# Optimization experiments

Measured on AMD Instinct MI355X. Metric: run time of the kernel, lower is better.

Reference implementation:

```python
import jax, jax.numpy as jnp
import numpy as np

N, DEG, C, D = 4096, 12, 4, 2
E = N * DEG
P = 2 * (D + 1) ** 2          # 18 radial MLPs: value set (s=0) + attention-key set (s=1)
R_MAX = (2 * D + 1) * C * C   # largest radial output size = 80


def _ln(x, g, b, eps=1e-5):
    mu = jnp.mean(x, axis=-1, keepdims=True)
    var = jnp.mean((x - mu) ** 2, axis=-1, keepdims=True)
    return (x - mu) / jnp.sqrt(var + eps) * g + b


def setup_inputs() -> dict:
    key = jax.random.key(0)
    ks = jax.random.split(key, 40)
    inp = {}
    inp["u"] = jax.random.randint(ks[0], (E,), 0, N)   # src nodes
    inp["v"] = jnp.repeat(jnp.arange(N), DEG)           # dst nodes: every node has DEG in-edges
    inp["dist"] = jax.random.uniform(ks[1], (E,))
    for k in range(D + 1):
        inp[f"f{k}"] = jax.random.normal(ks[2 + k], (N, C, 2 * k + 1))
    i = 5
    for k in range(D + 1):
        for l in range(D + 1):
            J = 2 * min(k, l) + 1
            inp[f"wj_{k}{l}"] = jax.random.normal(ks[i], (E, J, 2 * l + 1, 2 * k + 1)) * 0.2
            i += 1
    inp["wq"] = jax.random.normal(ks[i], (D + 1, C, C)) * 0.4; i += 1
    inp["rad_W1"] = jax.random.normal(ks[i], (P, 16, C + 1)) * 0.3; i += 1
    inp["rad_b1"] = jnp.zeros((P, 16)); inp["rad_g1"] = jnp.ones((P, 16)); inp["rad_be1"] = jnp.zeros((P, 16))
    inp["rad_W2"] = jax.random.normal(ks[i], (P, 16, 16)) * 0.25; i += 1
    inp["rad_b2"] = jnp.zeros((P, 16)); inp["rad_g2"] = jnp.ones((P, 16)); inp["rad_be2"] = jnp.zeros((P, 16))
    inp["rad_W3"] = jax.random.normal(ks[i], (P, R_MAX, 16)) * 0.2; i += 1
    inp["rad_b3"] = jnp.zeros((P, R_MAX))
    inp["si_W1"] = jax.random.normal(ks[i], (D + 1, C * C, C * C)) * 0.25; i += 1
    inp["si_b1"] = jnp.zeros((D + 1, C * C)); inp["si_g1"] = jnp.ones((D + 1, C * C)); inp["si_be1"] = jnp.zeros((D + 1, C * C))
    inp["si_W2"] = jax.random.normal(ks[i], (D + 1, C * C, C * C)) * 0.25; i += 1
    inp["si_b2"] = jnp.zeros((D + 1, C * C)); inp["si_g2"] = jnp.ones((D + 1, C * C)); inp["si_be2"] = jnp.zeros((D + 1, C * C))
    inp["si_W3"] = jax.random.normal(ks[i], (D + 1, C * C, C * C)) * 0.25; i += 1
    inp["si_b3"] = jnp.zeros((D + 1, C * C))
    return inp


def _forward(u, v, dist, f0, f1, f2,
             wj_00, wj_01, wj_02, wj_10, wj_11, wj_12, wj_20, wj_21, wj_22,
             wq, rad_W1, rad_b1, rad_g1, rad_be1, rad_W2, rad_b2, rad_g2, rad_be2, rad_W3, rad_b3,
             si_W1, si_b1, si_g1, si_be1, si_W2, si_b2, si_g2, si_be2, si_W3, si_b3):
    f = [f0, f1, f2]
    wj = {(0, 0): wj_00, (0, 1): wj_01, (0, 2): wj_02,
          (1, 0): wj_10, (1, 1): wj_11, (1, 2): wj_12,
          (2, 0): wj_20, (2, 1): wj_21, (2, 2): wj_22}
    n = f0.shape[0]
    # shared radial input: per-channel <f0_u, f0_v> plus edge distance -> [E, C+1]
    iv = jnp.concatenate([jnp.sum(f0[u] * f0[v], axis=2), dist[:, None]], axis=1)

    def radial(p, J):
        r_size = J * C * C
        h = jax.nn.relu(_ln(iv @ rad_W1[p].T + rad_b1[p], rad_g1[p], rad_be1[p]))
        h = jax.nn.relu(_ln(h @ rad_W2[p].T + rad_b2[p], rad_g2[p], rad_be2[p]))
        return h @ rad_W3[p, :r_size].T + rad_b3[p, :r_size]

    def make_w(k, l, s):
        # WLayer: radial MLP -> [E, J, c_out, c_in], contracted with CG basis w_j
        J = 2 * min(k, l) + 1
        p = s * (D + 1) ** 2 + k * (D + 1) + l
        Rm = radial(p, J).reshape(-1, J, C, C)
        return jnp.einsum('ejoi,ejlk->eoilk', Rm, wj[(k, l)])  # [E,o,i,2l+1,2k+1]

    # --- attention (AttnBlock) ---
    q = jnp.concatenate([jnp.einsum('oi,nik->nok', wq[k], f[k]) for k in range(D + 1)], axis=2)  # [N,C,9]
    k_edge = jnp.concatenate([
        sum(jnp.einsum('eoilk,eik->eol', make_w(k, l, 1), f[k][v]) for k in range(D + 1))
        for l in range(D + 1)], axis=2)  # [E,C,9] (keys use dst features, as in calc_k)
    dot = jnp.einsum('eol,eol->e', q[v], k_edge)
    m = jax.ops.segment_max(dot, v, num_segments=n)
    lse = m + jnp.log(jax.ops.segment_sum(jnp.exp(dot - m[v]), v, num_segments=n))
    a = jnp.exp(dot - lse[v])  # edge softmax over incoming edges of each dst node

    # --- attention-weighted tensor-product messages + scatter-sum (update_all) ---
    outs = []
    for l in range(D + 1):
        vl = sum(jnp.einsum('e,eoilk,eik->eol', a, make_w(k, l, 0), f[k][u]) for k in range(D + 1))
        outs.append(jax.ops.segment_sum(vl, v, num_segments=n))  # [N,C,2l+1]

    # --- self-interaction ---
    for l in range(D + 1):
        inner = jnp.einsum('ncl,ndl->ncd', f[l], f[l]).reshape(n, C * C)
        h = jax.nn.relu(_ln(inner @ si_W1[l].T + si_b1[l], si_g1[l], si_be1[l]))
        h = jax.nn.relu(_ln(h @ si_W2[l].T + si_b2[l], si_g2[l], si_be2[l]))
        siw = (h @ si_W3[l].T + si_b3[l]).reshape(n, C, C)
        outs[l] = outs[l] + jnp.einsum('noi,nil->nol', siw, f[l])

    # concat degree outputs f_out[0..2] along the m-axis -> [N, C, 1+3+5]
    return jnp.concatenate(outs, axis=2)


def reference(u, v, dist, f0, f1, f2,
              wj_00, wj_01, wj_02, wj_10, wj_11, wj_12, wj_20, wj_21, wj_22,
              wq, rad_W1, rad_b1, rad_g1, rad_be1, rad_W2, rad_b2, rad_g2, rad_be2, rad_W3, rad_b3,
              si_W1, si_b1, si_g1, si_be1, si_W2, si_b2, si_g2, si_be2, si_W3, si_b3):
    return _forward(u, v, dist, f0, f1, f2,
                    wj_00, wj_01, wj_02, wj_10, wj_11, wj_12, wj_20, wj_21, wj_22,
                    wq, rad_W1, rad_b1, rad_g1, rad_be1, rad_W2, rad_b2, rad_g2, rad_be2, rad_W3, rad_b3,
                    si_W1, si_b1, si_g1, si_be1, si_W2, si_b2, si_g2, si_be2, si_W3, si_b3)
```

## Files before the change

### kernel.cpp

```cpp
#include <hip/hip_runtime.h>
#include <hip/hip_bf16.h>

#define DEG 12

typedef short short8v __attribute__((ext_vector_type(8)));
typedef float float4v __attribute__((ext_vector_type(4)));

struct GP {
  const int* u;
  const void* dist;
  const void* f0; const void* f1; const void* f2;
  const void* wj[9];
  const void* wq;
  const void *rW1,*rb1,*rg1,*rbe1,*rW2,*rb2,*rg2,*rbe2,*rW3,*rb3;
  const void *sW1,*sb1,*sg1,*sbe1,*sW2,*sb2,*sg2,*sbe2,*sW3,*sb3;
  void* out;
  const float* wsf;
  const unsigned short* wA;
};

#define WS_W1   0
#define WS_W2   1440
#define WS_W3   6048
#define WS_SI1  29088
#define WS_SI2  29856
#define WS_SI3  30624
#define WS_G1   31392
#define WS_BE1  31680
#define WS_G2   31968
#define WS_BE2  32256
#define WS_B1   32544
#define WS_B2   32832
#define WS_B3   33120
#define WS_TOTAL 34560
#define WS_A_HALF 19456

struct alignas(16) Smem {
  float sRm[DEG][308];
  float sG[DEG][276];
  union {
    float sH2[DEG][148];
    unsigned short sB[9][4][16][4];
  };
  float sF[13][36];
  float sIv[DEG][5];
  float sQ[36];
  float sDot[DEG];
  float sA[DEG];
  float sVl[DEG][36];
  float sSIin[48], sSIh[48], sSIh2[48], sSiw[48];
};

__device__ __forceinline__ float ldv(const __hip_bfloat16* p, int i){ return __bfloat162float(p[i]); }
__device__ __forceinline__ float ldv(const float* p, int i){ return p[i]; }

__device__ __forceinline__ void load16(const __hip_bfloat16* ptr, float* out){
  const uint4* q = reinterpret_cast<const uint4*>(ptr);
  uint4 a = q[0]; uint4 b = q[1];
  unsigned w[8] = {a.x,a.y,a.z,a.w,b.x,b.y,b.z,b.w};
  #pragma unroll
  for (int i=0;i<8;i++){
    out[2*i]   = __uint_as_float(w[i] << 16);
    out[2*i+1] = __uint_as_float(w[i] & 0xffff0000u);
  }
}
__device__ __forceinline__ void load16(const float* ptr, float* out){
  const float4* q = reinterpret_cast<const float4*>(ptr);
  #pragma unroll
  for (int i=0;i<4;i++){
    float4 a = q[i];
    out[4*i]=a.x; out[4*i+1]=a.y; out[4*i+2]=a.z; out[4*i+3]=a.w;
  }
}

__device__ __forceinline__ void st(__hip_bfloat16* p, int i, float v){ p[i] = __float2bfloat16(v); }
__device__ __forceinline__ void st(float* p, int i, float v){ p[i] = v; }

__device__ __forceinline__ unsigned short f2bf(float v){
  __hip_bfloat16 b = __float2bfloat16(v);
  return *reinterpret_cast<unsigned short*>(&b);
}

template<typename WT>
__device__ __forceinline__ void ln_relu16(float* h, const WT* g, const WT* be){
  float mu = 0.f;
  #pragma unroll
  for (int c=0;c<16;c++) mu += h[c];
  mu *= 0.0625f;
  float var = 0.f;
  #pragma unroll
  for (int c=0;c<16;c++){ float d=h[c]-mu; var += d*d; }
  var *= 0.0625f;
  float inv = rsqrtf(var + 1e-5f);
  #pragma unroll
  for (int c=0;c<16;c++){
    float y = (h[c]-mu)*inv*ldv(g,c) + ldv(be,c);
    h[c] = fmaxf(y, 0.f);
  }
}

template<typename WT>
struct WPtr {
  const WT *w1,*w2,*w3,*si1,*si2,*si3,*g1,*be1,*g2,*be2,*b1,*b2,*b3;
};

template<typename WT>
__device__ __forceinline__ void radial12(int S, const WPtr<WT>& W, int t, Smem& s, bool mf){
  const int pk = t/12, e = t%12;
  const int pp = S*9 + pk;
  const float x0=s.sIv[e][0],x1=s.sIv[e][1],x2=s.sIv[e][2],x3=s.sIv[e][3],x4=s.sIv[e][4];
  float h[16];
  #pragma unroll
  for (int r=0;r<16;r++){
    const WT* row = W.w1 + (pp*16+r)*5;
    h[r] = ldv(W.b1,pp*16+r) + ldv(row,0)*x0 + ldv(row,1)*x1
         + ldv(row,2)*x2 + ldv(row,3)*x3 + ldv(row,4)*x4;
  }
  ln_relu16(h, W.g1+pp*16, W.be1+pp*16);
  float h2[16];
  #pragma unroll
  for (int r=0;r<16;r++){
    float wf[16]; load16(W.w2 + (pp*16+r)*16, wf);
    float acc = ldv(W.b2,pp*16+r);
    #pragma unroll
    for (int c=0;c<16;c++) acc += wf[c]*h[c];
    h2[r]=acc;
  }
  ln_relu16(h2, W.g2+pp*16, W.be2+pp*16);
  if (mf){
    #pragma unroll
    for (int c=0;c<16;c++) s.sB[pk][c>>2][e][c&3] = f2bf(h2[c]);
  } else {
    float4* dst = (float4*)&s.sH2[e][pk*16];
    #pragma unroll
    for (int i=0;i<4;i++) dst[i] = make_float4(h2[4*i],h2[4*i+1],h2[4*i+2],h2[4*i+3]);
  }
}

template<typename WT>
__device__ __forceinline__ void radial3(int S, const WPtr<WT>& W, int t, Smem& s){
  const int rq = t/3, eq = t%3;
  const int rflat = rq*4;
  constexpr int RS[10]={0,16,32,48,64,112,160,176,224,304};
  int kp=0;
  #pragma unroll
  for (int k=1;k<9;k++) if (rflat >= RS[k]) kp = k;
  const int rl = rflat - RS[kp];
  const int pp = S*9 + kp;
  const int wbase = (pp*80 + rl)*16;
  float b[4];
  #pragma unroll
  for (int r=0;r<4;r++) b[r] = ldv(W.b3, pp*80+rl+r);
  #pragma unroll
  for (int half=0; half<2; ++half){
    const int e0 = eq*4 + half*2, e1 = e0+1;
    const float4* hp0 = (const float4*)&s.sH2[e0][kp*16];
    const float4* hp1 = (const float4*)&s.sH2[e1][kp*16];
    float4 ha[4], hb[4];
    #pragma unroll
    for (int i=0;i<4;i++){ ha[i]=hp0[i]; hb[i]=hp1[i]; }
    float a0[4], a1[4];
    #pragma unroll
    for (int r=0;r<4;r++){
      float wf[16]; load16(W.w3 + wbase + r*16, wf);
      float s0=0.f, s1=0.f;
      const float* h0 = (const float*)&ha[0];
      const float* h1 = (const float*)&hb[0];
      #pragma unroll
      for (int c=0;c<16;c++){ s0 += wf[c]*h0[c]; s1 += wf[c]*h1[c]; }
      a0[r]=b[r]+s0; a1[r]=b[r]+s1;
    }
    *(float4*)&s.sRm[e0][rflat] = make_float4(a0[0],a0[1],a0[2],a0[3]);
    *(float4*)&s.sRm[e1][rflat] = make_float4(a1[0],a1[1],a1[2],a1[3]);
  }
}

__device__ __forceinline__ void radial3_mfma(int S, const float* wsf,
                                             const unsigned short* wA, int t, Smem& s){
  const int wave = t>>6, lane = t&63;
  const int col = lane&15, kq = lane>>4;
  #pragma unroll
  for (int t5=0; t5<5; ++t5){
    const int tile = wave + t5*4;
    if (tile < 19){
      const int rflat = tile*16;
      int kp=0;
      if (rflat>=16)  kp=1;
      if (rflat>=32)  kp=2;
      if (rflat>=48)  kp=3;
      if (rflat>=64)  kp=4;
      if (rflat>=112) kp=5;
      if (rflat>=160) kp=6;
      if (rflat>=176) kp=7;
      if (rflat>=224) kp=8;
      const int rs = (kp==0)?0:(kp==1)?16:(kp==2)?32:(kp==3)?48:(kp==4)?64:(kp==5)?112:(kp==6)?160:(kp==7)?176:224;
      const int rl = rflat - rs;
      const int pp = S*9 + kp;
      short8v a = *reinterpret_cast<const short8v*>(wA + (size_t)(S*19+tile)*512 + (size_t)lane*8);
      const unsigned short* bp = &s.sB[kp][kq][col][0];
      short4 blo = *reinterpret_cast<const short4*>(bp);
      short8v b;
      b[0]=blo.x; b[1]=blo.y; b[2]=blo.z; b[3]=blo.w;
      b[4]=blo.x; b[5]=blo.y; b[6]=blo.z; b[7]=blo.w;
      float4v c; c[0]=0.f; c[1]=0.f; c[2]=0.f; c[3]=0.f;
      float4v d = __builtin_amdgcn_mfma_f32_16x16x32_bf16(a, b, c, 0, 0, 0);
      if (col < 12){
        const float4 bb = *reinterpret_cast<const float4*>(wsf + WS_B3 + pp*80 + rl + kq*4);
        *(float4*)&s.sRm[col][rflat + kq*4] =
          make_float4(d[0]+bb.x, d[1]+bb.y, d[2]+bb.z, d[3]+bb.w);
      }
    }
  }
}

template<typename T>
__device__ __forceinline__ void stage_g(int S, const GP& p, int tt, int n12, Smem& s){
  constexpr int GOFF[9]={0,4,16,36,40,76,136,140,176};
  #pragma unroll
  for (int kp=0;kp<9;kp++){
    const int kk=kp/3, ll=kp%3;
    const int mn = kk<ll?kk:ll;
    const int J=2*mn+1, Lm=2*ll+1, Km=2*kk+1;
    const int koff = (kk==0)?0:((kk==1)?4:16);
    const int goff = GOFF[kp];
    const T* wjp = (const T*)p.wj[kp];
    const int nt = 12*J*Lm;
    for (int q=tt; q<nt; q+=128){
      int e = q/(J*Lm), jl = q%(J*Lm);
      int j = jl/Lm, lm = jl%Lm;
      const T* w = wjp + ((size_t)((n12+e)*J + j)*Lm + lm)*Km;
      const float* fv = S ? &s.sF[12][koff] : &s.sF[e][koff];
      float a0=0.f,a1=0.f,a2=0.f,a3=0.f;
      #pragma unroll
      for (int km=0;km<Km;km++){
        float wv = ldv(w,km);
        a0 += wv*fv[0*Km+km];
        a1 += wv*fv[1*Km+km];
        a2 += wv*fv[2*Km+km];
        a3 += wv*fv[3*Km+km];
      }
      float* gd = &s.sG[e][goff];
      gd[(j*4+0)*Lm+lm]=a0;
      gd[(j*4+1)*Lm+lm]=a1;
      gd[(j*4+2)*Lm+lm]=a2;
      gd[(j*4+3)*Lm+lm]=a3;
    }
  }
}

template<typename T, typename WT>
__device__ void gconv_run(const GP& p, Smem& s, const WPtr<WT>& W, bool mf){
  const int n = blockIdx.x;
  const int t = threadIdx.x;
  const int n12 = n*DEG;
  const T* f0=(const T*)p.f0; const T* f1=(const T*)p.f1; const T* f2=(const T*)p.f2;
  constexpr int ROFF[9]={0,16,32,48,64,112,160,176,224};
  constexpr int GOFF[9]={0,4,16,36,40,76,136,140,176};

  for (int q0=t; q0<13*36; q0+=256){
    int node=q0/36, j=q0%36;
    int idn = (node<DEG)? p.u[n12+node] : n;
    float v;
    if (j<4)       v = ldv(f0, idn*4  + j);
    else if (j<16) v = ldv(f1, idn*12 + (j-4));
    else           v = ldv(f2, idn*20 + (j-16));
    s.sF[node][j] = v;
  }
  __syncthreads();

  if (t<48){ int e=t>>2, c=t&3; s.sIv[e][c] = s.sF[e][c]*s.sF[12][c]; }
  else if (t<60){ int e=t-48; s.sIv[e][4] = ldv((const T*)p.dist, n12+e); }
  else if (t>=64 && t<100){
    int t2=t-64, o=t2/9, mc=t2%9;
    int k = (mc<1)?0:((mc<4)?1:2);
    int m = mc - ((k==0)?0:((k==1)?1:4));
    int koff=(k==0)?0:((k==1)?4:16), Km=2*k+1;
    float acc=0.f;
    #pragma unroll
    for (int i=0;i<4;i++) acc += ldv((const T*)p.wq,(k*4+o)*4+i) * s.sF[12][koff+i*Km+m];
    s.sQ[t2]=acc;
  } else if (t>=128 && t<176){
    int t3=t-128, l=t3/16, rr=t3%16, o=rr>>2, i=rr&3;
    int koff=(l==0)?0:((l==1)?4:16), Lm=2*l+1;
    float acc=0.f;
    for (int m=0;m<Lm;m++) acc += s.sF[12][koff+o*Lm+m]*s.sF[12][koff+i*Lm+m];
    s.sSIin[t3]=acc;
  }
  __syncthreads();

  if (t<108)       radial12(1, W, t, s, mf);
  else if (t>=128) stage_g<T>(1, p, t-128, n12, s);
  __syncthreads();

  if (mf)          radial3_mfma(1, p.wsf, p.wA, t, s);
  else if (t<228)  radial3(1, W, t, s);
  __syncthreads();

  if (t<192){
    const int e=t>>4, o=(t>>2)&3, i=t&3;
    float d=0.f;
    #pragma unroll
    for (int kp=0;kp<9;kp++){
      const int kk=kp/3, ll=kp%3;
      const int mn=kk<ll?kk:ll;
      const int J=2*mn+1, Lm=2*ll+1;
      const int loff=(ll==0)?0:((ll==1)?1:4);
      #pragma unroll
      for (int j=0;j<J;j++){
        float rm = s.sRm[e][ROFF[kp]+j*16+o*4+i];
        #pragma unroll
        for (int lm=0;lm<Lm;lm++)
          d += rm * s.sG[e][GOFF[kp]+(j*4+i)*Lm+lm] * s.sQ[o*9+loff+lm];
      }
    }
    d += __shfl_xor(d,1);
    d += __shfl_xor(d,2);
    d += __shfl_xor(d,4);
    d += __shfl_xor(d,8);
    if ((t&15)==0) s.sDot[e]=d;
  } else if (t<240){
    int idx=t-192, l=idx/16, r=idx%16;
    float wf[16]; load16(W.si1 + (l*16+r)*16, wf);
    float acc = ldv((const T*)p.sb1,l*16+r);
    #pragma unroll
    for (int c=0;c<16;c++) acc += wf[c]*s.sSIin[l*16+c];
    s.sSIh[idx]=acc;
  }
  __syncthreads();

  if (t<108)       radial12(0, W, t, s, mf);
  else if (t==127){
    float mx=-1e30f;
    #pragma unroll
    for (int e=0;e<12;e++) mx = fmaxf(mx, s.sDot[e]);
    float ex[12]; float se=0.f;
    #pragma unroll
    for (int e=0;e<12;e++){ ex[e]=__expf(s.sDot[e]-mx); se += ex[e]; }
    #pragma unroll
    for (int e=0;e<12;e++) s.sA[e] = ex[e]/se;
  }
  else if (t>=128) stage_g<T>(0, p, t-128, n12, s);
  __syncthreads();

  if (mf)          radial3_mfma(0, p.wsf, p.wA, t, s);
  else if (t<228)  radial3(0, W, t, s);
  __syncthreads();

  if (t>=64){
    for (int q=t-64; q<432; q+=192){
      int l,e,o,lm;
      if (q<48){ l=0; e=q>>2; o=q&3; lm=0; }
      else if (q<192){ int r=q-48; l=1; e=r/12; int r2=r%12; o=r2/3; lm=r2%3; }
      else { int r=q-192; l=2; e=r/20; int r2=r%20; o=r2/5; lm=r2%5; }
      const int Lm=2*l+1, loff=(l==0)?0:((l==1)?1:4);
      float acc=0.f;
      for (int kk=0;kk<3;kk++){
        const int kp=kk*3+l;
        const int mn=kk<l?kk:l;
        const int J=2*mn+1;
        for (int j=0;j<J;j++)
          #pragma unroll
          for (int i=0;i<4;i++)
            acc += s.sRm[e][ROFF[kp]+j*16+o*4+i] * s.sG[e][GOFF[kp]+(j*4+i)*Lm+lm];
      }
      s.sVl[e][o*9+loff+lm]=acc;
    }
  } else if (t<48){
    int l=t/16, r=t%16;
    float mu=0.f;
    #pragma unroll
    for (int c=0;c<16;c++) mu += s.sSIh[l*16+c];
    mu *= 0.0625f;
    float var=0.f;
    #pragma unroll
    for (int c=0;c<16;c++){ float d=s.sSIh[l*16+c]-mu; var+=d*d; }
    var *= 0.0625f;
    float inv = rsqrtf(var+1e-5f);
    float wf[16]; load16(W.si2 + (l*16+r)*16, wf);
    float acc = ldv((const T*)p.sb2,l*16+r);
    #pragma unroll
    for (int c=0;c<16;c++){
      float y = (s.sSIh[l*16+c]-mu)*inv*ldv((const T*)p.sg1,l*16+c) + ldv((const T*)p.sbe1,l*16+c);
      acc += wf[c]*fmaxf(y,0.f);
    }
    s.sSIh2[t]=acc;
  }
  __syncthreads();

  if (t<48){
    int l=t/16, r=t%16;
    float mu=0.f;
    #pragma unroll
    for (int c=0;c<16;c++) mu += s.sSIh2[l*16+c];
    mu *= 0.0625f;
    float var=0.f;
    #pragma unroll
    for (int c=0;c<16;c++){ float d=s.sSIh2[l*16+c]-mu; var+=d*d; }
    var *= 0.0625f;
    float inv = rsqrtf(var+1e-5f);
    float wf[16]; load16(W.si3 + (l*16+r)*16, wf);
    float acc = ldv((const T*)p.sb3,l*16+r);
    #pragma unroll
    for (int c=0;c<16;c++){
      float y = (s.sSIh2[l*16+c]-mu)*inv*ldv((const T*)p.sg2,l*16+c) + ldv((const T*)p.sbe2,l*16+c);
      acc += wf[c]*fmaxf(y,0.f);
    }
    s.sSiw[t]=acc;
  }
  __syncthreads();

  if (t<36){
    int o=t/9, mc=t%9;
    int l = (mc<1)?0:((mc<4)?1:2);
    int m = mc - ((l==0)?0:((l==1)?1:4));
    int koff=(l==0)?0:((l==1)?4:16), Lm=2*l+1;
    float acc=0.f;
    #pragma unroll
    for (int e=0;e<12;e++) acc += s.sA[e]*s.sVl[e][t];
    #pragma unroll
    for (int i=0;i<4;i++) acc += s.sSiw[l*16+o*4+i]*s.sF[12][koff+i*Lm+m];
    st((T*)p.out, n*36+t, acc);
  }
}

template<typename T>
__device__ __forceinline__ void gconv_dispatch(const GP& p, Smem& s){
  if (p.wsf){
    const float* w = p.wsf;
    WPtr<float> W{w+WS_W1, w+WS_W2, w+WS_W3, w+WS_SI1, w+WS_SI2, w+WS_SI3,
                  w+WS_G1, w+WS_BE1, w+WS_G2, w+WS_BE2, w+WS_B1, w+WS_B2, w+WS_B3};
    gconv_run<T,float>(p, s, W, p.wA != nullptr);
  } else {
    WPtr<T> W{(const T*)p.rW1,(const T*)p.rW2,(const T*)p.rW3,
              (const T*)p.sW1,(const T*)p.sW2,(const T*)p.sW3,
              (const T*)p.rg1,(const T*)p.rbe1,(const T*)p.rg2,(const T*)p.rbe2,
              (const T*)p.rb1,(const T*)p.rb2,(const T*)p.rb3};
    gconv_run<T,T>(p, s, W, false);
  }
}

__global__ __launch_bounds__(256,4) void gconv_kernel(GP p){
  __shared__ Smem s;
  const unsigned magic = *(const unsigned*)p.rg1;
  if (magic == 0x3F803F80u) gconv_dispatch<__hip_bfloat16>(p, s);
  else                      gconv_dispatch<float>(p, s);
}

template<typename T>
__device__ __forceinline__ void prep_body(const GP& p, float* ws, int i){
  float v;
  if      (i<WS_W2)  v = ldv((const T*)p.rW1,  i-WS_W1);
  else if (i<WS_W3)  v = ldv((const T*)p.rW2,  i-WS_W2);
  else if (i<WS_SI1) v = ldv((const T*)p.rW3,  i-WS_W3);
  else if (i<WS_SI2) v = ldv((const T*)p.sW1,  i-WS_SI1);
  else if (i<WS_SI3) v = ldv((const T*)p.sW2,  i-WS_SI2);
  else if (i<WS_G1)  v = ldv((const T*)p.sW3,  i-WS_SI3);
  else if (i<WS_BE1) v = ldv((const T*)p.rg1,  i-WS_G1);
  else if (i<WS_G2)  v = ldv((const T*)p.rbe1, i-WS_BE1);
  else if (i<WS_BE2) v = ldv((const T*)p.rg2,  i-WS_G2);
  else if (i<WS_B1)  v = ldv((const T*)p.rbe2, i-WS_BE2);
  else if (i<WS_B2)  v = ldv((const T*)p.rb1,  i-WS_B1);
  else if (i<WS_B3)  v = ldv((const T*)p.rb2,  i-WS_B2);
  else               v = ldv((const T*)p.rb3,  i-WS_B3);
  ws[i] = v;
}

__global__ void prep_kernel(GP p, float* ws){
  int i = blockIdx.x*256 + threadIdx.x;
  if (i >= WS_TOTAL) return;
  const unsigned magic = *(const unsigned*)p.rg1;
  if (magic == 0x3F803F80u) prep_body<__hip_bfloat16>(p, ws, i);
  else                      prep_body<float>(p, ws, i);
}

__global__ void prep2_kernel(GP p, unsigned short* wsA){
  int i = blockIdx.x*256 + threadIdx.x;
  if (i >= 2*19*512) return;
  const unsigned magic = *(const unsigned*)p.rg1;
  int st   = i>>9;
  int lane = (i>>3)&63;
  int j    = i&7;
  int S = st/19, tile = st%19;
  int rflat = tile*16;
  int kp=0;
  if (rflat>=16)  kp=1;
  if (rflat>=32)  kp=2;
  if (rflat>=48)  kp=3;
  if (rflat>=64)  kp=4;
  if (rflat>=112) kp=5;
  if (rflat>=160) kp=6;
  if (rflat>=176) kp=7;
  if (rflat>=224) kp=8;
  const int rs = (kp==0)?0:(kp==1)?16:(kp==2)?32:(kp==3)?48:(kp==4)?64:(kp==5)?112:(kp==6)?160:(kp==7)?176:224;
  const int rl = rflat - rs;
  const int pp = S*9 + kp;
  const int row = lane&15;
  const int k = 4*(lane>>4) + (j&3);
  float v = 0.f;
  if (j < 4){
    int idx = (pp*80 + rl + row)*16 + k;
    v = (magic==0x3F803F80u) ? ldv((const __hip_bfloat16*)p.rW3, idx)
                             : ldv((const float*)p.rW3, idx);
  }
  wsA[i] = f2bf(v);
}

extern "C" void kernel_launch(void* const* d_in, const int* in_sizes, int n_in,
                              void* d_out, int out_size, void* d_ws, size_t ws_size,
                              hipStream_t stream) {
  GP p;
  p.u    = (const int*)d_in[0];
  p.dist = d_in[2];
  p.f0   = d_in[3];
  p.f1   = d_in[4];
  p.f2   = d_in[5];
  for (int kp=0;kp<9;kp++) p.wj[kp] = d_in[6+kp];
  p.wq   = d_in[15];
  p.rW1  = d_in[16]; p.rb1  = d_in[17]; p.rg1  = d_in[18]; p.rbe1 = d_in[19];
  p.rW2  = d_in[20]; p.rb2  = d_in[21]; p.rg2  = d_in[22]; p.rbe2 = d_in[23];
  p.rW3  = d_in[24]; p.rb3  = d_in[25];
  p.sW1  = d_in[26]; p.sb1  = d_in[27]; p.sg1  = d_in[28]; p.sbe1 = d_in[29];
  p.sW2  = d_in[30]; p.sb2  = d_in[31]; p.sg2  = d_in[32]; p.sbe2 = d_in[33];
  p.sW3  = d_in[34]; p.sb3  = d_in[35];
  p.out  = d_out;

  const bool use_ws = (ws_size >= (size_t)WS_TOTAL*sizeof(float));
  const bool use_mf = (ws_size >= (size_t)WS_TOTAL*sizeof(float) + (size_t)WS_A_HALF*sizeof(unsigned short));
  p.wsf = use_ws ? (const float*)d_ws : nullptr;
  unsigned short* wsA = use_mf ? (unsigned short*)((float*)d_ws + WS_TOTAL) : nullptr;
  p.wA = wsA;

  if (use_ws)
    prep_kernel<<<dim3((WS_TOTAL+255)/256), dim3(256), 0, stream>>>(p, (float*)d_ws);
  if (use_mf)
    prep2_kernel<<<dim3((2*19*512+255)/256), dim3(256), 0, stream>>>(p, wsA);
  gconv_kernel<<<dim3(4096), dim3(256), 0, stream>>>(p);
}
```

Before: 258.5 us.

## Fuse radial MFMA output with attention-dot and value contraction, split MFMA kernel

Adds a separate MFMA-path kernel that no longer writes the radial weights to shared memory. It contracts the MFMA results directly with the basis products in registers, accumulating the attention logits (key set) and the per-edge values (value set) with LDS atomics. The self-interaction MLP steps are spread across otherwise idle threads of the existing stages, which removes separate passes and barriers. Dropping the large sRm and sH2 buffers shrinks the shared-memory footprint, which may allow more resident blocks, at the cost of LDS atomic contention and a duplicated fallback kernel.

```diff
diff --git a/kernel.cpp b/kernel.cpp
--- a/kernel.cpp
+++ b/kernel.cpp
@@ -35,20 +35,16 @@
 #define WS_TOTAL 34560
 #define WS_A_HALF 19456
 
-struct alignas(16) Smem {
-  float sRm[DEG][308];
+struct alignas(16) SmemM {
   float sG[DEG][276];
-  union {
-    float sH2[DEG][148];
-    unsigned short sB[9][4][16][4];
-  };
   float sF[13][36];
+  float sVl[DEG][36];
   float sIv[DEG][5];
   float sQ[36];
   float sDot[DEG];
   float sA[DEG];
-  float sVl[DEG][36];
-  float sSIin[48], sSIh[48], sSIh2[48], sSiw[48];
+  float sSIa[48], sSIb[48];
+  unsigned short sB[2][9][4][16][4];
 };
 
 __device__ __forceinline__ float ldv(const __hip_bfloat16* p, int i){ return __bfloat162float(p[i]); }
@@ -104,81 +100,38 @@
   const WT *w1,*w2,*w3,*si1,*si2,*si3,*g1,*be1,*g2,*be2,*b1,*b2,*b3;
 };
 
-template<typename WT>
-__device__ __forceinline__ void radial12(int S, const WPtr<WT>& W, int t, Smem& s, bool mf){
+
+__device__ __forceinline__ void radial12m(int S, const WPtr<float>& W, int t, SmemM& s){
   const int pk = t/12, e = t%12;
   const int pp = S*9 + pk;
   const float x0=s.sIv[e][0],x1=s.sIv[e][1],x2=s.sIv[e][2],x3=s.sIv[e][3],x4=s.sIv[e][4];
   float h[16];
   #pragma unroll
   for (int r=0;r<16;r++){
-    const WT* row = W.w1 + (pp*16+r)*5;
-    h[r] = ldv(W.b1,pp*16+r) + ldv(row,0)*x0 + ldv(row,1)*x1
-         + ldv(row,2)*x2 + ldv(row,3)*x3 + ldv(row,4)*x4;
+    const float* row = W.w1 + (pp*16+r)*5;
+    h[r] = W.b1[pp*16+r] + row[0]*x0 + row[1]*x1 + row[2]*x2 + row[3]*x3 + row[4]*x4;
   }
   ln_relu16(h, W.g1+pp*16, W.be1+pp*16);
   float h2[16];
   #pragma unroll
   for (int r=0;r<16;r++){
     float wf[16]; load16(W.w2 + (pp*16+r)*16, wf);
-    float acc = ldv(W.b2,pp*16+r);
+    float acc = W.b2[pp*16+r];
     #pragma unroll
     for (int c=0;c<16;c++) acc += wf[c]*h[c];
     h2[r]=acc;
   }
   ln_relu16(h2, W.g2+pp*16, W.be2+pp*16);
-  if (mf){
-    #pragma unroll
-    for (int c=0;c<16;c++) s.sB[pk][c>>2][e][c&3] = f2bf(h2[c]);
-  } else {
-    float4* dst = (float4*)&s.sH2[e][pk*16];
-    #pragma unroll
-    for (int i=0;i<4;i++) dst[i] = make_float4(h2[4*i],h2[4*i+1],h2[4*i+2],h2[4*i+3]);
-  }
-}
-
-template<typename WT>
-__device__ __forceinline__ void radial3(int S, const WPtr<WT>& W, int t, Smem& s){
-  const int rq = t/3, eq = t%3;
-  const int rflat = rq*4;
-  constexpr int RS[10]={0,16,32,48,64,112,160,176,224,304};
-  int kp=0;
-  #pragma unroll
-  for (int k=1;k<9;k++) if (rflat >= RS[k]) kp = k;
-  const int rl = rflat - RS[kp];
-  const int pp = S*9 + kp;
-  const int wbase = (pp*80 + rl)*16;
-  float b[4];
-  #pragma unroll
-  for (int r=0;r<4;r++) b[r] = ldv(W.b3, pp*80+rl+r);
-  #pragma unroll
-  for (int half=0; half<2; ++half){
-    const int e0 = eq*4 + half*2, e1 = e0+1;
-    const float4* hp0 = (const float4*)&s.sH2[e0][kp*16];
-    const float4* hp1 = (const float4*)&s.sH2[e1][kp*16];
-    float4 ha[4], hb[4];
-    #pragma unroll
-    for (int i=0;i<4;i++){ ha[i]=hp0[i]; hb[i]=hp1[i]; }
-    float a0[4], a1[4];
-    #pragma unroll
-    for (int r=0;r<4;r++){
-      float wf[16]; load16(W.w3 + wbase + r*16, wf);
-      float s0=0.f, s1=0.f;
-      const float* h0 = (const float*)&ha[0];
-      const float* h1 = (const float*)&hb[0];
-      #pragma unroll
-      for (int c=0;c<16;c++){ s0 += wf[c]*h0[c]; s1 += wf[c]*h1[c]; }
-      a0[r]=b[r]+s0; a1[r]=b[r]+s1;
-    }
-    *(float4*)&s.sRm[e0][rflat] = make_float4(a0[0],a0[1],a0[2],a0[3]);
-    *(float4*)&s.sRm[e1][rflat] = make_float4(a1[0],a1[1],a1[2],a1[3]);
-  }
-}
-
-__device__ __forceinline__ void radial3_mfma(int S, const float* wsf,
-                                             const unsigned short* wA, int t, Smem& s){
+  #pragma unroll
+  for (int c=0;c<16;c++) s.sB[S][pk][c>>2][e][c&3] = f2bf(h2[c]);
+}
+
+template<int S>
+__device__ __forceinline__ void radial3_fused(const float* wsf, const unsigned short* wA,
+                                              int t, SmemM& s){
   const int wave = t>>6, lane = t&63;
   const int col = lane&15, kq = lane>>4;
+  float dotAcc = 0.f;
   #pragma unroll
   for (int t5=0; t5<5; ++t5){
     const int tile = wave + t5*4;
@@ -193,28 +146,54 @@
       if (rflat>=160) kp=6;
       if (rflat>=176) kp=7;
       if (rflat>=224) kp=8;
-      const int rs = (kp==0)?0:(kp==1)?16:(kp==2)?32:(kp==3)?48:(kp==4)?64:(kp==5)?112:(kp==6)?160:(kp==7)?176:224;
+      const int rs  = (kp==0)?0:(kp==1)?16:(kp==2)?32:(kp==3)?48:(kp==4)?64:(kp==5)?112:(kp==6)?160:(kp==7)?176:224;
+      const int gof = (kp==0)?0:(kp==1)?4:(kp==2)?16:(kp==3)?36:(kp==4)?40:(kp==5)?76:(kp==6)?136:(kp==7)?140:176;
+      const int ll  = (kp==0||kp==3||kp==6)?0:((kp==1||kp==4||kp==7)?1:2);
       const int rl = rflat - rs;
+      const int j  = rl>>4;
       const int pp = S*9 + kp;
+      const int Lm = 2*ll+1;
+      const int loff = (ll==0)?0:((ll==1)?1:4);
+
       short8v a = *reinterpret_cast<const short8v*>(wA + (size_t)(S*19+tile)*512 + (size_t)lane*8);
-      const unsigned short* bp = &s.sB[kp][kq][col][0];
+      const unsigned short* bp = &s.sB[S][kp][kq][col][0];
       short4 blo = *reinterpret_cast<const short4*>(bp);
       short8v b;
       b[0]=blo.x; b[1]=blo.y; b[2]=blo.z; b[3]=blo.w;
       b[4]=blo.x; b[5]=blo.y; b[6]=blo.z; b[7]=blo.w;
       float4v c; c[0]=0.f; c[1]=0.f; c[2]=0.f; c[3]=0.f;
       float4v d = __builtin_amdgcn_mfma_f32_16x16x32_bf16(a, b, c, 0, 0, 0);
+
       if (col < 12){
         const float4 bb = *reinterpret_cast<const float4*>(wsf + WS_B3 + pp*80 + rl + kq*4);
-        *(float4*)&s.sRm[col][rflat + kq*4] =
-          make_float4(d[0]+bb.x, d[1]+bb.y, d[2]+bb.z, d[3]+bb.w);
+        const float r0 = d[0]+bb.x, r1 = d[1]+bb.y, r2 = d[2]+bb.z, r3 = d[3]+bb.w;
+        const float* g0 = &s.sG[col][gof + (j*4)*Lm];
+        if (S==1){
+          #pragma unroll
+          for (int lm=0; lm<5; lm++){
+            if (lm<Lm){
+              float q = s.sQ[kq*9+loff+lm];
+              float u = r0*g0[lm] + r1*g0[Lm+lm] + r2*g0[2*Lm+lm] + r3*g0[3*Lm+lm];
+              dotAcc += q*u;
+            }
+          }
+        } else {
+          #pragma unroll
+          for (int lm=0; lm<5; lm++){
+            if (lm<Lm){
+              float u = r0*g0[lm] + r1*g0[Lm+lm] + r2*g0[2*Lm+lm] + r3*g0[3*Lm+lm];
+              atomicAdd(&s.sVl[col][kq*9+loff+lm], u);
+            }
+          }
+        }
       }
     }
   }
-}
-
-template<typename T>
-__device__ __forceinline__ void stage_g(int S, const GP& p, int tt, int n12, Smem& s){
+  if (S==1 && col<12) atomicAdd(&s.sDot[col], dotAcc);
+}
+
+template<typename T, typename SM>
+__device__ __forceinline__ void stage_g(int S, const GP& p, int tt, int n12, SM& s){
   constexpr int GOFF[9]={0,4,16,36,40,76,136,140,176};
   #pragma unroll
   for (int kp=0;kp<9;kp++){
@@ -248,14 +227,12 @@
   }
 }
 
-template<typename T, typename WT>
-__device__ void gconv_run(const GP& p, Smem& s, const WPtr<WT>& W, bool mf){
+template<typename T>
+__device__ void gconv_mf_run(const GP& p, SmemM& s, const WPtr<float>& W){
   const int n = blockIdx.x;
   const int t = threadIdx.x;
   const int n12 = n*DEG;
   const T* f0=(const T*)p.f0; const T* f1=(const T*)p.f1; const T* f2=(const T*)p.f2;
-  constexpr int ROFF[9]={0,16,32,48,64,112,160,176,224};
-  constexpr int GOFF[9]={0,4,16,36,40,76,136,140,176};
 
   for (int q0=t; q0<13*36; q0+=256){
     int node=q0/36, j=q0%36;
@@ -266,6 +243,8 @@
     else           v = ldv(f2, idn*20 + (j-16));
     s.sF[node][j] = v;
   }
+  for (int q=t; q<432; q+=256) (&s.sVl[0][0])[q]=0.f;
+  if (t<12) s.sDot[t]=0.f;
   __syncthreads();
 
   if (t<48){ int e=t>>2, c=t&3; s.sIv[e][c] = s.sF[e][c]*s.sF[12][c]; }
@@ -284,16 +263,236 @@
     int koff=(l==0)?0:((l==1)?4:16), Lm=2*l+1;
     float acc=0.f;
     for (int m=0;m<Lm;m++) acc += s.sF[12][koff+o*Lm+m]*s.sF[12][koff+i*Lm+m];
+    s.sSIa[t3]=acc;
+  }
+  __syncthreads();
+
+  if (t<108) radial12m(1, W, t, s);
+  else if (t<128){
+    for (int q=t-108; q<48; q+=20){
+      int l=q/16, r=q%16;
+      float wf[16]; load16(W.si1 + (l*16+r)*16, wf);
+      float acc = ldv((const T*)p.sb1,l*16+r);
+      #pragma unroll
+      for (int c=0;c<16;c++) acc += wf[c]*s.sSIa[l*16+c];
+      s.sSIb[q]=acc;
+    }
+  }
+  else stage_g<T>(1, p, t-128, n12, s);
+  __syncthreads();
+
+  radial3_fused<1>(p.wsf, p.wA, t, s);
+  __syncthreads();
+
+  if (t<108) radial12m(0, W, t, s);
+  else if (t<127){
+    for (int q=t-108; q<48; q+=19){
+      int l=q/16, r=q%16;
+      float mu=0.f;
+      #pragma unroll
+      for (int c=0;c<16;c++) mu += s.sSIb[l*16+c];
+      mu *= 0.0625f;
+      float var=0.f;
+      #pragma unroll
+      for (int c=0;c<16;c++){ float d=s.sSIb[l*16+c]-mu; var+=d*d; }
+      var *= 0.0625f;
+      float inv = rsqrtf(var+1e-5f);
+      float wf[16]; load16(W.si2 + (l*16+r)*16, wf);
+      float acc = ldv((const T*)p.sb2,l*16+r);
+      #pragma unroll
+      for (int c=0;c<16;c++){
+        float y = (s.sSIb[l*16+c]-mu)*inv*ldv((const T*)p.sg1,l*16+c) + ldv((const T*)p.sbe1,l*16+c);
+        acc += wf[c]*fmaxf(y,0.f);
+      }
+      s.sSIa[q]=acc;
+    }
+  }
+  else if (t==127){
+    float mx=-1e30f;
+    #pragma unroll
+    for (int e=0;e<12;e++) mx = fmaxf(mx, s.sDot[e]);
+    float ex[12]; float se=0.f;
+    #pragma unroll
+    for (int e=0;e<12;e++){ ex[e]=__expf(s.sDot[e]-mx); se += ex[e]; }
+    #pragma unroll
+    for (int e=0;e<12;e++) s.sA[e] = ex[e]/se;
+  }
+  else stage_g<T>(0, p, t-128, n12, s);
+  __syncthreads();
+
+  radial3_fused<0>(p.wsf, p.wA, t, s);
+  __syncthreads();
+
+  if (t<48){
+    int l=t/16, r=t%16;
+    float mu=0.f;
+    #pragma unroll
+    for (int c=0;c<16;c++) mu += s.sSIa[l*16+c];
+    mu *= 0.0625f;
+    float var=0.f;
+    #pragma unroll
+    for (int c=0;c<16;c++){ float d=s.sSIa[l*16+c]-mu; var+=d*d; }
+    var *= 0.0625f;
+    float inv = rsqrtf(var+1e-5f);
+    float wf[16]; load16(W.si3 + (l*16+r)*16, wf);
+    float acc = ldv((const T*)p.sb3,l*16+r);
+    #pragma unroll
+    for (int c=0;c<16;c++){
+      float y = (s.sSIa[l*16+c]-mu)*inv*ldv((const T*)p.sg2,l*16+c) + ldv((const T*)p.sbe2,l*16+c);
+      acc += wf[c]*fmaxf(y,0.f);
+    }
+    s.sSIb[t]=acc;
+  }
+  __syncthreads();
+
+  if (t<36){
+    int o=t/9, mc=t%9;
+    int l = (mc<1)?0:((mc<4)?1:2);
+    int m = mc - ((l==0)?0:((l==1)?1:4));
+    int koff=(l==0)?0:((l==1)?4:16), Lm=2*l+1;
+    float acc=0.f;
+    #pragma unroll
+    for (int e=0;e<12;e++) acc += s.sA[e]*s.sVl[e][t];
+    #pragma unroll
+    for (int i=0;i<4;i++) acc += s.sSIb[l*16+o*4+i]*s.sF[12][koff+i*Lm+m];
+    st((T*)p.out, n*36+t, acc);
+  }
+}
+
+__global__ __launch_bounds__(256,4) void gconv_mf(GP p){
+  __shared__ SmemM s;
+  const float* w = p.wsf;
+  WPtr<float> W{w+WS_W1, w+WS_W2, w+WS_W3, w+WS_SI1, w+WS_SI2, w+WS_SI3,
+                w+WS_G1, w+WS_BE1, w+WS_G2, w+WS_BE2, w+WS_B1, w+WS_B2, w+WS_B3};
+  const unsigned magic = *(const unsigned*)p.rg1;
+  if (magic == 0x3F803F80u) gconv_mf_run<__hip_bfloat16>(p, s, W);
+  else                      gconv_mf_run<float>(p, s, W);
+}
+
+struct alignas(16) SmemF {
+  float sRm[DEG][308];
+  float sG[DEG][276];
+  float sH2[DEG][148];
+  float sF[13][36];
+  float sIv[DEG][5];
+  float sQ[36];
+  float sDot[DEG];
+  float sA[DEG];
+  float sVl[DEG][36];
+  float sSIin[48], sSIh[48], sSIh2[48], sSiw[48];
+};
+
+template<typename WT>
+__device__ __forceinline__ void radial12f(int S, const WPtr<WT>& W, int t, SmemF& s){
+  const int pk = t/12, e = t%12;
+  const int pp = S*9 + pk;
+  const float x0=s.sIv[e][0],x1=s.sIv[e][1],x2=s.sIv[e][2],x3=s.sIv[e][3],x4=s.sIv[e][4];
+  float h[16];
+  #pragma unroll
+  for (int r=0;r<16;r++){
+    const WT* row = W.w1 + (pp*16+r)*5;
+    h[r] = ldv(W.b1,pp*16+r) + ldv(row,0)*x0 + ldv(row,1)*x1
+         + ldv(row,2)*x2 + ldv(row,3)*x3 + ldv(row,4)*x4;
+  }
+  ln_relu16(h, W.g1+pp*16, W.be1+pp*16);
+  float h2[16];
+  #pragma unroll
+  for (int r=0;r<16;r++){
+    float wf[16]; load16(W.w2 + (pp*16+r)*16, wf);
+    float acc = ldv(W.b2,pp*16+r);
+    #pragma unroll
+    for (int c=0;c<16;c++) acc += wf[c]*h[c];
+    h2[r]=acc;
+  }
+  ln_relu16(h2, W.g2+pp*16, W.be2+pp*16);
+  float4* dst = (float4*)&s.sH2[e][pk*16];
+  #pragma unroll
+  for (int i=0;i<4;i++) dst[i] = make_float4(h2[4*i],h2[4*i+1],h2[4*i+2],h2[4*i+3]);
+}
+
+template<typename WT>
+__device__ __forceinline__ void radial3f(int S, const WPtr<WT>& W, int t, SmemF& s){
+  const int rq = t/3, eq = t%3;
+  const int rflat = rq*4;
+  constexpr int RS[10]={0,16,32,48,64,112,160,176,224,304};
+  int kp=0;
+  #pragma unroll
+  for (int k=1;k<9;k++) if (rflat >= RS[k]) kp = k;
+  const int rl = rflat - RS[kp];
+  const int pp = S*9 + kp;
+  const int wbase = (pp*80 + rl)*16;
+  float b[4];
+  #pragma unroll
+  for (int r=0;r<4;r++) b[r] = ldv(W.b3, pp*80+rl+r);
+  #pragma unroll
+  for (int half=0; half<2; ++half){
+    const int e0 = eq*4 + half*2, e1 = e0+1;
+    const float4* hp0 = (const float4*)&s.sH2[e0][kp*16];
+    const float4* hp1 = (const float4*)&s.sH2[e1][kp*16];
+    float4 ha[4], hb[4];
+    #pragma unroll
+    for (int i=0;i<4;i++){ ha[i]=hp0[i]; hb[i]=hp1[i]; }
+    float a0[4], a1[4];
+    #pragma unroll
+    for (int r=0;r<4;r++){
+      float wf[16]; load16(W.w3 + wbase + r*16, wf);
+      float s0=0.f, s1=0.f;
+      const float* h0 = (const float*)&ha[0];
+      const float* h1 = (const float*)&hb[0];
+      #pragma unroll
+      for (int c=0;c<16;c++){ s0 += wf[c]*h0[c]; s1 += wf[c]*h1[c]; }
+      a0[r]=b[r]+s0; a1[r]=b[r]+s1;
+    }
+    *(float4*)&s.sRm[e0][rflat] = make_float4(a0[0],a0[1],a0[2],a0[3]);
+    *(float4*)&s.sRm[e1][rflat] = make_float4(a1[0],a1[1],a1[2],a1[3]);
+  }
+}
+
+template<typename T, typename WT>
+__device__ void gconv_fb_run(const GP& p, SmemF& s, const WPtr<WT>& W){
+  const int n = blockIdx.x;
+  const int t = threadIdx.x;
+  const int n12 = n*DEG;
+  const T* f0=(const T*)p.f0; const T* f1=(const T*)p.f1; const T* f2=(const T*)p.f2;
+  constexpr int ROFF[9]={0,16,32,48,64,112,160,176,224};
+  constexpr int GOFF[9]={0,4,16,36,40,76,136,140,176};
+
+  for (int q0=t; q0<13*36; q0+=256){
+    int node=q0/36, j=q0%36;
+    int idn = (node<DEG)? p.u[n12+node] : n;
+    float v;
+    if (j<4)       v = ldv(f0, idn*4  + j);
+    else if (j<16) v = ldv(f1, idn*12 + (j-4));
+    else           v = ldv(f2, idn*20 + (j-16));
+    s.sF[node][j] = v;
+  }
+  __syncthreads();
+
+  if (t<48){ int e=t>>2, c=t&3; s.sIv[e][c] = s.sF[e][c]*s.sF[12][c]; }
+  else if (t<60){ int e=t-48; s.sIv[e][4] = ldv((const T*)p.dist, n12+e); }
+  else if (t>=64 && t<100){
+    int t2=t-64, o=t2/9, mc=t2%9;
+    int k = (mc<1)?0:((mc<4)?1:2);
+    int m = mc - ((k==0)?0:((k==1)?1:4));
+    int koff=(k==0)?0:((k==1)?4:16), Km=2*k+1;
+    float acc=0.f;
+    #pragma unroll
+    for (int i=0;i<4;i++) acc += ldv((const T*)p.wq,(k*4+o)*4+i) * s.sF[12][koff+i*Km+m];
+    s.sQ[t2]=acc;
+  } else if (t>=128 && t<176){
+    int t3=t-128, l=t3/16, rr=t3%16, o=rr>>2, i=rr&3;
+    int koff=(l==0)?0:((l==1)?4:16), Lm=2*l+1;
+    float acc=0.f;
+    for (int m=0;m<Lm;m++) acc += s.sF[12][koff+o*Lm+m]*s.sF[12][koff+i*Lm+m];
     s.sSIin[t3]=acc;
   }
   __syncthreads();
 
-  if (t<108)       radial12(1, W, t, s, mf);
+  if (t<108)       radial12f(1, W, t, s);
   else if (t>=128) stage_g<T>(1, p, t-128, n12, s);
   __syncthreads();
 
-  if (mf)          radial3_mfma(1, p.wsf, p.wA, t, s);
-  else if (t<228)  radial3(1, W, t, s);
+  if (t<228) radial3f(1, W, t, s);
   __syncthreads();
 
   if (t<192){
@@ -328,7 +527,7 @@
   }
   __syncthreads();
 
-  if (t<108)       radial12(0, W, t, s, mf);
+  if (t<108)       radial12f(0, W, t, s);
   else if (t==127){
     float mx=-1e30f;
     #pragma unroll
@@ -342,8 +541,7 @@
   else if (t>=128) stage_g<T>(0, p, t-128, n12, s);
   __syncthreads();
 
-  if (mf)          radial3_mfma(0, p.wsf, p.wA, t, s);
-  else if (t<228)  radial3(0, W, t, s);
+  if (t<228) radial3f(0, W, t, s);
   __syncthreads();
 
   if (t>=64){
@@ -423,27 +621,28 @@
   }
 }
 
-template<typename T>
-__device__ __forceinline__ void gconv_dispatch(const GP& p, Smem& s){
+__global__ __launch_bounds__(256,4) void gconv_fb(GP p){
+  __shared__ SmemF s;
+  const unsigned magic = *(const unsigned*)p.rg1;
   if (p.wsf){
     const float* w = p.wsf;
     WPtr<float> W{w+WS_W1, w+WS_W2, w+WS_W3, w+WS_SI1, w+WS_SI2, w+WS_SI3,
                   w+WS_G1, w+WS_BE1, w+WS_G2, w+WS_BE2, w+WS_B1, w+WS_B2, w+WS_B3};
-    gconv_run<T,float>(p, s, W, p.wA != nullptr);
+    if (magic == 0x3F803F80u) gconv_fb_run<__hip_bfloat16,float>(p, s, W);
+    else                      gconv_fb_run<float,float>(p, s, W);
+  } else if (magic == 0x3F803F80u){
+    WPtr<__hip_bfloat16> W{(const __hip_bfloat16*)p.rW1,(const __hip_bfloat16*)p.rW2,(const __hip_bfloat16*)p.rW3,
+              (const __hip_bfloat16*)p.sW1,(const __hip_bfloat16*)p.sW2,(const __hip_bfloat16*)p.sW3,
+              (const __hip_bfloat16*)p.rg1,(const __hip_bfloat16*)p.rbe1,(const __hip_bfloat16*)p.rg2,(const __hip_bfloat16*)p.rbe2,
+              (const __hip_bfloat16*)p.rb1,(const __hip_bfloat16*)p.rb2,(const __hip_bfloat16*)p.rb3};
+    gconv_fb_run<__hip_bfloat16,__hip_bfloat16>(p, s, W);
   } else {
-    WPtr<T> W{(const T*)p.rW1,(const T*)p.rW2,(const T*)p.rW3,
-              (const T*)p.sW1,(const T*)p.sW2,(const T*)p.sW3,
-              (const T*)p.rg1,(const T*)p.rbe1,(const T*)p.rg2,(const T*)p.rbe2,
-              (const T*)p.rb1,(const T*)p.rb2,(const T*)p.rb3};
-    gconv_run<T,T>(p, s, W, false);
-  }
-}
-
-__global__ __launch_bounds__(256,4) void gconv_kernel(GP p){
-  __shared__ Smem s;
-  const unsigned magic = *(const unsigned*)p.rg1;
-  if (magic == 0x3F803F80u) gconv_dispatch<__hip_bfloat16>(p, s);
-  else                      gconv_dispatch<float>(p, s);
+    WPtr<float> W{(const float*)p.rW1,(const float*)p.rW2,(const float*)p.rW3,
+              (const float*)p.sW1,(const float*)p.sW2,(const float*)p.sW3,
+              (const float*)p.rg1,(const float*)p.rbe1,(const float*)p.rg2,(const float*)p.rbe2,
+              (const float*)p.rb1,(const float*)p.rb2,(const float*)p.rb3};
+    gconv_fb_run<float,float>(p, s, W);
+  }
 }
 
 template<typename T>
@@ -532,7 +731,10 @@
 
   if (use_ws)
     prep_kernel<<<dim3((WS_TOTAL+255)/256), dim3(256), 0, stream>>>(p, (float*)d_ws);
-  if (use_mf)
+  if (use_mf){
     prep2_kernel<<<dim3((2*19*512+255)/256), dim3(256), 0, stream>>>(p, wsA);
-  gconv_kernel<<<dim3(4096), dim3(256), 0, stream>>>(p);
-}
+    gconv_mf<<<dim3(4096), dim3(256), 0, stream>>>(p);
+  } else {
+    gconv_fb<<<dim3(4096), dim3(256), 0, stream>>>(p);
+  }
+}
```

Measured after the change: 313.8 us. +21.4%, slower.
